# Performance work log

Hardware: AMD Instinct MI355X
Metric: run time of the kernel (lower is better)

Reference implementation:

```python
import jax, jax.numpy as jnp
import numpy as np

DATA_NUM = 1024
CLS_NUM = 32000


def setup_inputs() -> dict:
    key = jax.random.key(0)
    k1, k2, k3, k4 = jax.random.split(key, 4)
    h1 = jax.random.normal(k1, (DATA_NUM, 2), dtype=jnp.float32) + 3.0
    e1 = jax.random.normal(k2, (CLS_NUM, 2), dtype=jnp.float32)
    h3 = jax.random.normal(k3, (DATA_NUM, 2), dtype=jnp.float32) * 2.0
    e3 = jax.random.normal(k4, (CLS_NUM, 2), dtype=jnp.float32)
    return {"h1": h1, "e1": e1, "h3": h3, "e3": e3, "share_head": 0}


def cal_akl(l1, l2):
    # l1: student logits (D, C); l2: teacher logits (D, C)
    probs1 = jax.nn.softmax(l1, axis=-1)
    probs2 = jax.nn.softmax(l2, axis=-1)
    # sort teacher probs ascending; gather student probs in same order
    sorted_idx = jnp.argsort(probs2, axis=-1)
    sorted_probs2 = jnp.take_along_axis(probs2, sorted_idx, axis=-1)
    sorted_probs1 = jnp.take_along_axis(probs1, sorted_idx, axis=-1)
    gap = jnp.abs(sorted_probs2 - sorted_probs1)
    cum_probs2 = jnp.cumsum(sorted_probs2, axis=-1)
    tail_mask = (cum_probs2 < 0.5).astype(l1.dtype)
    g_head = jax.lax.stop_gradient(jnp.sum(gap * (1.0 - tail_mask), axis=-1))
    g_tail = jax.lax.stop_gradient(jnp.sum(gap * tail_mask, axis=-1))
    lprobs1 = jax.nn.log_softmax(l1, axis=-1)
    lprobs2 = jax.nn.log_softmax(l2, axis=-1)
    fkl = jnp.sum(probs2 * (lprobs2 - lprobs1), axis=-1)
    rkl = jnp.sum(probs1 * (lprobs1 - lprobs2), axis=-1)
    denom = g_head + g_tail
    akl = (g_head / denom) * fkl + (g_tail / denom) * rkl
    return jnp.mean(akl)


def reference(h1, e1, h3, e3, share_head):
    # share_head is a static Python int/bool; obj == 'akl', share_head == 0 path
    if share_head:
        raise NotImplementedError("reference covers share_head=False path")
    stu_logits = h1 @ e1.T   # (D, C)
    tea_logits = h3 @ e3.T   # (D, C)
    return cal_akl(stu_logits, tea_logits)
```

## Files before the change

### kernel.cpp

```cpp
#include <hip/hip_runtime.h>
#include <math.h>

#define DNUM 1024
#define CNUM 32000
#define NT 512
#define R 2
#define GRID (DNUM / R)
#define KC 4
#define KF 8
#define NQ (CNUM / 4)
#define NFULL (NQ / NT)
#define TAILN (NQ - NFULL*NT)

#define L2E 1.4426950408889634f
#define LN2 0.6931471805599453f

typedef float v2f __attribute__((ext_vector_type(2)));

__device__ __forceinline__ v2f splat2(float s) { v2f v; v.x = s; v.y = s; return v; }

__device__ __forceinline__ float wave_red_sum(float v) {
    #pragma unroll
    for (int o = 32; o > 0; o >>= 1) v += __shfl_down(v, o, 64);
    return v;
}

__global__ __launch_bounds__(NT, 4) void akl_rows(
    const float* __restrict__ h1, const float* __restrict__ e1,
    const float* __restrict__ h3, const float* __restrict__ e3,
    float* __restrict__ out)
{
    const int tid  = threadIdx.x;
    const int lane = tid & 63, wid = tid >> 6;
    const int row0 = blockIdx.x * R;

    __shared__ float pool[16384];
    __shared__ float red[48];
    __shared__ float shCS[R*KC];
    __shared__ float shFP[R*KF], shFG[R*KF];
    __shared__ float shA[R][7];

    float a1L[R], b1L[R], a2L[R], b2L[R], mh1L[R], mh2L[R], icwC[R], c0C[R];
    #pragma unroll
    for (int r = 0; r < R; r++) {
        a1L[r] = h1[2*(row0+r)] * L2E; b1L[r] = h1[2*(row0+r)+1] * L2E;
        a2L[r] = h3[2*(row0+r)] * L2E; b2L[r] = h3[2*(row0+r)+1] * L2E;
        mh1L[r] = 6.0f * (fabsf(a1L[r]) + fabsf(b1L[r]));
        mh2L[r] = 6.0f * (fabsf(a2L[r]) + fabsf(b2L[r]));
        float sp = fmaxf(sqrtf(a2L[r]*a2L[r] + b2L[r]*b2L[r]), 1e-6f);
        icwC[r] = 1.0f / (1.35f * sp);
        c0C[r] = 0.5f/1.35f + mh2L[r]*icwC[r];
    }
    for (int i = tid; i < 16384; i += NT) pool[i] = 0.f;
    __syncthreads();

    const float4* __restrict__ E1 = (const float4*)e1;
    const float4* __restrict__ E3 = (const float4*)e3;

    v2f U1v[R], S1v[R], S2v[R];
    #pragma unroll
    for (int r = 0; r < R; r++) { U1v[r] = splat2(0.f); S1v[r] = splat2(0.f); S2v[r] = splat2(0.f); }

    auto body1 = [&](int j) {
        float4 A0 = E1[2*j], A1 = E1[2*j+1], B0 = E3[2*j], B1 = E3[2*j+1];
        #pragma unroll
        for (int r = 0; r < R; r++) {
            const v2f a1v = splat2(a1L[r]), b1v = splat2(b1L[r]);
            const v2f a2v = splat2(a2L[r]), b2v = splat2(b2L[r]);
            const v2f m1v = splat2(-mh1L[r]), m2v = splat2(-mh2L[r]);
            const v2f icv = splat2(icwC[r]), c0v = splat2(c0C[r]);
            #pragma unroll
            for (int p = 0; p < 2; p++) {
                float4 A = p ? A1 : A0, B = p ? B1 : B0;
                v2f X1; X1.x = A.x; X1.y = A.z;
                v2f Y1; Y1.x = A.y; Y1.y = A.w;
                v2f X3; X3.x = B.x; X3.y = B.z;
                v2f Y3; Y3.x = B.y; Y3.y = B.w;
                v2f l1 = a1v*X1 + (b1v*Y1 + m1v);
                v2f l2 = a2v*X3 + (b2v*Y3 + m2v);
                v2f e1v; e1v.x = __builtin_amdgcn_exp2f(l1.x);
                         e1v.y = __builtin_amdgcn_exp2f(l1.y);
                v2f e2v; e2v.x = __builtin_amdgcn_exp2f(l2.x);
                         e2v.y = __builtin_amdgcn_exp2f(l2.y);
                v2f dp = l2 - l1;
                U1v[r] += e1v;
                S1v[r] += e1v * dp;
                S2v[r] += e2v * dp;
                v2f t = l2*icv + c0v;
                float t0 = fminf(fmaxf(t.x, 0.f), 3.f);
                float t1 = fminf(fmaxf(t.y, 0.f), 3.f);
                int b0 = (int)t0, b1i = (int)t1;
                float* H0 = pool + (r*4 + 2*p    )*2048;
                float* H1 = pool + (r*4 + 2*p + 1)*2048;
                H0[b0*NT + tid]  += e2v.x;
                H1[b1i*NT + tid] += e2v.y;
            }
        }
    };
    #pragma unroll 1
    for (int it = 0; it < NFULL; ++it) body1(it*NT + tid);
    if (tid < TAILN) body1(NFULL*NT + tid);

    #pragma unroll
    for (int r = 0; r < R; r++) {
        float u = wave_red_sum(U1v[r].x + U1v[r].y);
        float s1 = wave_red_sum(S1v[r].x + S1v[r].y);
        float s2 = wave_red_sum(S2v[r].x + S2v[r].y);
        if (lane == 0) {
            red[wid*6 + r*3 + 0] = u;
            red[wid*6 + r*3 + 1] = s1;
            red[wid*6 + r*3 + 2] = s2;
        }
    }
    __syncthreads();

    {
        int grp = tid >> 6, l = tid & 63;
        int r = grp >> 2, b = grp & 3;
        float s = 0.f;
        #pragma unroll
        for (int c = 0; c < 4; c++) {
            const float* H = pool + (r*4 + c)*2048 + b*512;
            #pragma unroll
            for (int t = 0; t < 8; t++) s += H[l + t*64];
        }
        s = wave_red_sum(s);
        if (l == 0) shCS[grp] = s;
    }
    __syncthreads();

    if (tid < R) {
        const int r = tid;
        float U1s = 0, S1s = 0, S2s = 0;
        for (int w = 0; w < 8; w++) {
            U1s += red[w*6 + r*3 + 0];
            S1s += red[w*6 + r*3 + 1];
            S2s += red[w*6 + r*3 + 2];
        }
        float U2s = 0.f;
        #pragma unroll
        for (int i = 0; i < KC; i++) U2s += shCS[r*KC + i];
        float mh1r = r ? mh1L[1] : mh1L[0];
        float mh2r = r ? mh2L[1] : mh2L[0];
        float a2r = r ? a2L[1] : a2L[0];
        float b2r = r ? b2L[1] : b2L[0];
        float dmh = mh2r - mh1r;
        S1s += dmh * U1s;
        S2s += dmh * U2s;
        float M1 = mh1r + __builtin_amdgcn_logf(U1s);
        float M2 = mh2r + __builtin_amdgcn_logf(U2s);
        float delta = M2 - M1;
        float thr = 0.5f * U2s;
        float S = 0.f; int bsel = KC-1;
        for (int i = 0; i < KC; i++) {
            float m = shCS[r*KC + i];
            if (S + m >= thr) { bsel = i; break; }
            S += m;
        }
        float sp = fmaxf(sqrtf(a2r*a2r + b2r*b2r), 1e-6f);
        float wc  = 1.35f * sp;
        float loS_s = fmaf((float)bsel, wc, -0.5f*sp) - mh2r;
        float icwF = (float)KF / wc;
        shA[r][0] = U2s / U1s;
        shA[r][1] = thr;
        shA[r][2] = LN2 * (S2s/U2s - delta);
        shA[r][3] = LN2 * (delta - S1s/U1s);
        shA[r][4] = icwF;
        shA[r][5] = -loS_s * icwF;
        shA[r][6] = S;
    }
    for (int i = tid; i < 16384; i += NT) pool[i] = 0.f;
    __syncthreads();

    float cR[R], icwFl[R], c0Fl[R];
    #pragma unroll
    for (int r = 0; r < R; r++) {
        cR[r] = shA[r][0]; icwFl[r] = shA[r][4]; c0Fl[r] = shA[r][5];
    }
    v2f gtv[R], Gpv[R];
    #pragma unroll
    for (int r = 0; r < R; r++) { gtv[r] = splat2(0.f); Gpv[r] = splat2(0.f); }

    auto body2 = [&](int j) {
        float4 A0 = E1[2*j], A1 = E1[2*j+1], B0 = E3[2*j], B1 = E3[2*j+1];
        #pragma unroll
        for (int r = 0; r < R; r++) {
            const v2f a1v = splat2(a1L[r]), b1v = splat2(b1L[r]);
            const v2f a2v = splat2(a2L[r]), b2v = splat2(b2L[r]);
            const v2f m1v = splat2(-mh1L[r]), m2v = splat2(-mh2L[r]);
            const v2f cv = splat2(-cR[r]);
            const v2f icv = splat2(icwFl[r]), c0v = splat2(c0Fl[r]);
            float* HP = pool + r*4096;
            float* HG = pool + (2+r)*4096;
            #pragma unroll
            for (int p = 0; p < 2; p++) {
                float4 A = p ? A1 : A0, B = p ? B1 : B0;
                v2f X1; X1.x = A.x; X1.y = A.z;
                v2f Y1; Y1.x = A.y; Y1.y = A.w;
                v2f X3; X3.x = B.x; X3.y = B.z;
                v2f Y3; Y3.x = B.y; Y3.y = B.w;
                v2f l1 = a1v*X1 + (b1v*Y1 + m1v);
                v2f l2 = a2v*X3 + (b2v*Y3 + m2v);
                v2f e1v; e1v.x = __builtin_amdgcn_exp2f(l1.x);
                         e1v.y = __builtin_amdgcn_exp2f(l1.y);
                v2f e2v; e2v.x = __builtin_amdgcn_exp2f(l2.x);
                         e2v.y = __builtin_amdgcn_exp2f(l2.y);
                v2f d = cv*e1v + e2v;
                v2f gap; gap.x = fabsf(d.x); gap.y = fabsf(d.y);
                gtv[r] += gap;
                v2f t = l2*icv + c0v;
                Gpv[r].x += (t.x < 0.f) ? gap.x : 0.f;
                Gpv[r].y += (t.y < 0.f) ? gap.y : 0.f;
                if (t.x >= 0.f && t.x < (float)KF) {
                    int fb = (int)t.x;
                    HP[fb*NT + tid] += e2v.x;
                    HG[fb*NT + tid] += gap.x;
                }
                if (t.y >= 0.f && t.y < (float)KF) {
                    int fb = (int)t.y;
                    HP[fb*NT + tid] += e2v.y;
                    HG[fb*NT + tid] += gap.y;
                }
            }
        }
    };
    #pragma unroll 1
    for (int it = 0; it < NFULL; ++it) body2(it*NT + tid);
    if (tid < TAILN) body2(NFULL*NT + tid);

    #pragma unroll
    for (int r = 0; r < R; r++) {
        float a = wave_red_sum(gtv[r].x + gtv[r].y);
        float b = wave_red_sum(Gpv[r].x + Gpv[r].y);
        if (lane == 0) { red[wid*4 + r*2 + 0] = a; red[wid*4 + r*2 + 1] = b; }
    }
    __syncthreads();

    {
        int grp = tid >> 4, l16 = tid & 15;
        int isG = grp >> 4;
        int r = (grp >> 3) & 1, b = grp & 7;
        const float* H = pool + (isG*2 + r)*4096 + b*512;
        float s = 0.f;
        #pragma unroll
        for (int t = 0; t < NT/16; t++) s += H[l16 + t*16];
        #pragma unroll
        for (int o = 8; o > 0; o >>= 1) s += __shfl_down(s, o, 64);
        if (l16 == 0) {
            if (isG) shFG[r*KF + b] = s; else shFP[r*KF + b] = s;
        }
    }
    __syncthreads();

    if (tid < R) {
        const int r = tid;
        float gts = 0, Gp = 0;
        for (int w = 0; w < 8; w++) {
            gts += red[w*4 + r*2 + 0];
            Gp  += red[w*4 + r*2 + 1];
        }
        float thr = shA[r][1], fkl = shA[r][2], rkl = shA[r][3];
        float S = shA[r][6], G = Gp;
        bool done = false;
        #pragma unroll
        for (int i = 0; i < KF; i++) {
            if (!done) {
                float p = shFP[r*KF + i], g = shFG[r*KF + i];
                float ns = S + p;
                if (ns >= thr) {
                    float f = (thr - S) / fmaxf(p, 1e-30f);
                    f = fminf(fmaxf(f, 0.f), 1.f);
                    G += f * g;
                    done = true;
                } else { S = ns; G += g; }
            }
        }
        float gl = G;
        float gh = gts - gl;
        float akl = (gh*fkl + gl*rkl) / gts;
        unsafeAtomicAdd(out, akl * (1.0f/(float)DNUM));
    }
}

extern "C" void kernel_launch(void* const* d_in, const int* in_sizes, int n_in,
                              void* d_out, int out_size, void* d_ws, size_t ws_size,
                              hipStream_t stream) {
    const float* h1 = (const float*)d_in[0];
    const float* e1 = (const float*)d_in[1];
    const float* h3 = (const float*)d_in[2];
    const float* e3 = (const float*)d_in[3];
    hipMemsetAsync(d_out, 0, sizeof(float), stream);
    akl_rows<<<GRID, NT, 0, stream>>>(h1, e1, h3, e3, (float*)d_out);
}
```

Measured before the change: 107.1 us.

## Process one row per block instead of two, halving LDS and raising occupancy

Each block now handles a single data row instead of two, so the grid doubles to one block per row. Shared-memory histograms shrink from 64KB to 32KB and launch bounds rise to allow more resident blocks per CU. The tail iteration is folded into the main loop count. The cost is that the e1/e3 class tables are streamed twice as many times overall, since the two rows no longer share each load.

```diff
diff --git a/kernel.cpp b/kernel.cpp
--- a/kernel.cpp
+++ b/kernel.cpp
@@ -4,8 +4,7 @@
 #define DNUM 1024
 #define CNUM 32000
 #define NT 512
-#define R 2
-#define GRID (DNUM / R)
+#define GRID DNUM
 #define KC 4
 #define KF 8
 #define NQ (CNUM / 4)
@@ -25,50 +24,49 @@
     return v;
 }
 
-__global__ __launch_bounds__(NT, 4) void akl_rows(
+__global__ __launch_bounds__(NT, 8) void akl_rows(
     const float* __restrict__ h1, const float* __restrict__ e1,
     const float* __restrict__ h3, const float* __restrict__ e3,
     float* __restrict__ out)
 {
     const int tid  = threadIdx.x;
     const int lane = tid & 63, wid = tid >> 6;
-    const int row0 = blockIdx.x * R;
-
-    __shared__ float pool[16384];
-    __shared__ float red[48];
-    __shared__ float shCS[R*KC];
-    __shared__ float shFP[R*KF], shFG[R*KF];
-    __shared__ float shA[R][7];
-
-    float a1L[R], b1L[R], a2L[R], b2L[R], mh1L[R], mh2L[R], icwC[R], c0C[R];
-    #pragma unroll
-    for (int r = 0; r < R; r++) {
-        a1L[r] = h1[2*(row0+r)] * L2E; b1L[r] = h1[2*(row0+r)+1] * L2E;
-        a2L[r] = h3[2*(row0+r)] * L2E; b2L[r] = h3[2*(row0+r)+1] * L2E;
-        mh1L[r] = 6.0f * (fabsf(a1L[r]) + fabsf(b1L[r]));
-        mh2L[r] = 6.0f * (fabsf(a2L[r]) + fabsf(b2L[r]));
-        float sp = fmaxf(sqrtf(a2L[r]*a2L[r] + b2L[r]*b2L[r]), 1e-6f);
-        icwC[r] = 1.0f / (1.35f * sp);
-        c0C[r] = 0.5f/1.35f + mh2L[r]*icwC[r];
-    }
-    for (int i = tid; i < 16384; i += NT) pool[i] = 0.f;
+    const int row = blockIdx.x;
+
+    __shared__ float pool[8192];
+    __shared__ float red[24];
+    __shared__ float shCS[KC];
+    __shared__ float shFP[KF], shFG[KF];
+    __shared__ float shA[7];
+
+    const float a1L = h1[2*row] * L2E,  b1L = h1[2*row+1] * L2E;
+    const float a2L = h3[2*row] * L2E,  b2L = h3[2*row+1] * L2E;
+    const float mh1L = 6.0f * (fabsf(a1L) + fabsf(b1L));
+    const float mh2L = 6.0f * (fabsf(a2L) + fabsf(b2L));
+    const float spC = fmaxf(sqrtf(a2L*a2L + b2L*b2L), 1e-6f);
+    const float icwC = 1.0f / (1.35f * spC);
+    const float c0C = 0.5f/1.35f + mh2L*icwC;
+
+    for (int i = tid; i < 8192; i += NT) pool[i] = 0.f;
     __syncthreads();
 
     const float4* __restrict__ E1 = (const float4*)e1;
     const float4* __restrict__ E3 = (const float4*)e3;
 
-    v2f U1v[R], S1v[R], S2v[R];
-    #pragma unroll
-    for (int r = 0; r < R; r++) { U1v[r] = splat2(0.f); S1v[r] = splat2(0.f); S2v[r] = splat2(0.f); }
-
-    auto body1 = [&](int j) {
-        float4 A0 = E1[2*j], A1 = E1[2*j+1], B0 = E3[2*j], B1 = E3[2*j+1];
-        #pragma unroll
-        for (int r = 0; r < R; r++) {
-            const v2f a1v = splat2(a1L[r]), b1v = splat2(b1L[r]);
-            const v2f a2v = splat2(a2L[r]), b2v = splat2(b2L[r]);
-            const v2f m1v = splat2(-mh1L[r]), m2v = splat2(-mh2L[r]);
-            const v2f icv = splat2(icwC[r]), c0v = splat2(c0C[r]);
+    const int cnt = NFULL + ((tid < TAILN) ? 1 : 0);
+
+    v2f U1v = splat2(0.f), S1v = splat2(0.f), S2v = splat2(0.f);
+
+    {
+        const v2f a1v = splat2(a1L), b1v = splat2(b1L);
+        const v2f a2v = splat2(a2L), b2v = splat2(b2L);
+        const v2f m1v = splat2(-mh1L), m2v = splat2(-mh2L);
+        const v2f icv = splat2(icwC), c0v = splat2(c0C);
+        #pragma unroll 1
+        for (int it = 0; it < cnt; ++it) {
+            const int j = it*NT + tid;
+            float4 A0 = E1[2*j], A1 = E1[2*j+1];
+            float4 B0 = E3[2*j], B1 = E3[2*j+1];
             #pragma unroll
             for (int p = 0; p < 2; p++) {
                 float4 A = p ? A1 : A0, B = p ? B1 : B0;
@@ -83,115 +81,100 @@
                 v2f e2v; e2v.x = __builtin_amdgcn_exp2f(l2.x);
                          e2v.y = __builtin_amdgcn_exp2f(l2.y);
                 v2f dp = l2 - l1;
-                U1v[r] += e1v;
-                S1v[r] += e1v * dp;
-                S2v[r] += e2v * dp;
+                U1v += e1v;
+                S1v += e1v * dp;
+                S2v += e2v * dp;
                 v2f t = l2*icv + c0v;
                 float t0 = fminf(fmaxf(t.x, 0.f), 3.f);
                 float t1 = fminf(fmaxf(t.y, 0.f), 3.f);
                 int b0 = (int)t0, b1i = (int)t1;
-                float* H0 = pool + (r*4 + 2*p    )*2048;
-                float* H1 = pool + (r*4 + 2*p + 1)*2048;
+                float* H0 = pool + (2*p    )*2048;
+                float* H1 = pool + (2*p + 1)*2048;
                 H0[b0*NT + tid]  += e2v.x;
                 H1[b1i*NT + tid] += e2v.y;
             }
         }
-    };
-    #pragma unroll 1
-    for (int it = 0; it < NFULL; ++it) body1(it*NT + tid);
-    if (tid < TAILN) body1(NFULL*NT + tid);
-
-    #pragma unroll
-    for (int r = 0; r < R; r++) {
-        float u = wave_red_sum(U1v[r].x + U1v[r].y);
-        float s1 = wave_red_sum(S1v[r].x + S1v[r].y);
-        float s2 = wave_red_sum(S2v[r].x + S2v[r].y);
+    }
+
+    {
+        float u  = wave_red_sum(U1v.x + U1v.y);
+        float s1 = wave_red_sum(S1v.x + S1v.y);
+        float s2 = wave_red_sum(S2v.x + S2v.y);
         if (lane == 0) {
-            red[wid*6 + r*3 + 0] = u;
-            red[wid*6 + r*3 + 1] = s1;
-            red[wid*6 + r*3 + 2] = s2;
-        }
-    }
-    __syncthreads();
-
-    {
-        int grp = tid >> 6, l = tid & 63;
-        int r = grp >> 2, b = grp & 3;
+            red[wid*3 + 0] = u;
+            red[wid*3 + 1] = s1;
+            red[wid*3 + 2] = s2;
+        }
+    }
+    __syncthreads();
+
+    if (tid < 256) {
+        int b = tid >> 6, l = tid & 63;
         float s = 0.f;
         #pragma unroll
         for (int c = 0; c < 4; c++) {
-            const float* H = pool + (r*4 + c)*2048 + b*512;
+            const float* H = pool + c*2048 + b*512;
             #pragma unroll
             for (int t = 0; t < 8; t++) s += H[l + t*64];
         }
         s = wave_red_sum(s);
-        if (l == 0) shCS[grp] = s;
-    }
-    __syncthreads();
-
-    if (tid < R) {
-        const int r = tid;
+        if (l == 0) shCS[b] = s;
+    }
+    __syncthreads();
+
+    if (tid == 0) {
         float U1s = 0, S1s = 0, S2s = 0;
         for (int w = 0; w < 8; w++) {
-            U1s += red[w*6 + r*3 + 0];
-            S1s += red[w*6 + r*3 + 1];
-            S2s += red[w*6 + r*3 + 2];
+            U1s += red[w*3 + 0];
+            S1s += red[w*3 + 1];
+            S2s += red[w*3 + 2];
         }
         float U2s = 0.f;
         #pragma unroll
-        for (int i = 0; i < KC; i++) U2s += shCS[r*KC + i];
-        float mh1r = r ? mh1L[1] : mh1L[0];
-        float mh2r = r ? mh2L[1] : mh2L[0];
-        float a2r = r ? a2L[1] : a2L[0];
-        float b2r = r ? b2L[1] : b2L[0];
-        float dmh = mh2r - mh1r;
+        for (int i = 0; i < KC; i++) U2s += shCS[i];
+        float dmh = mh2L - mh1L;
         S1s += dmh * U1s;
         S2s += dmh * U2s;
-        float M1 = mh1r + __builtin_amdgcn_logf(U1s);
-        float M2 = mh2r + __builtin_amdgcn_logf(U2s);
+        float M1 = mh1L + __builtin_amdgcn_logf(U1s);
+        float M2 = mh2L + __builtin_amdgcn_logf(U2s);
         float delta = M2 - M1;
         float thr = 0.5f * U2s;
         float S = 0.f; int bsel = KC-1;
         for (int i = 0; i < KC; i++) {
-            float m = shCS[r*KC + i];
+            float m = shCS[i];
             if (S + m >= thr) { bsel = i; break; }
             S += m;
         }
-        float sp = fmaxf(sqrtf(a2r*a2r + b2r*b2r), 1e-6f);
-        float wc  = 1.35f * sp;
-        float loS_s = fmaf((float)bsel, wc, -0.5f*sp) - mh2r;
+        float wc  = 1.35f * spC;
+        float loS_s = fmaf((float)bsel, wc, -0.5f*spC) - mh2L;
         float icwF = (float)KF / wc;
-        shA[r][0] = U2s / U1s;
-        shA[r][1] = thr;
-        shA[r][2] = LN2 * (S2s/U2s - delta);
-        shA[r][3] = LN2 * (delta - S1s/U1s);
-        shA[r][4] = icwF;
-        shA[r][5] = -loS_s * icwF;
-        shA[r][6] = S;
-    }
-    for (int i = tid; i < 16384; i += NT) pool[i] = 0.f;
-    __syncthreads();
-
-    float cR[R], icwFl[R], c0Fl[R];
-    #pragma unroll
-    for (int r = 0; r < R; r++) {
-        cR[r] = shA[r][0]; icwFl[r] = shA[r][4]; c0Fl[r] = shA[r][5];
-    }
-    v2f gtv[R], Gpv[R];
-    #pragma unroll
-    for (int r = 0; r < R; r++) { gtv[r] = splat2(0.f); Gpv[r] = splat2(0.f); }
-
-    auto body2 = [&](int j) {
-        float4 A0 = E1[2*j], A1 = E1[2*j+1], B0 = E3[2*j], B1 = E3[2*j+1];
-        #pragma unroll
-        for (int r = 0; r < R; r++) {
-            const v2f a1v = splat2(a1L[r]), b1v = splat2(b1L[r]);
-            const v2f a2v = splat2(a2L[r]), b2v = splat2(b2L[r]);
-            const v2f m1v = splat2(-mh1L[r]), m2v = splat2(-mh2L[r]);
-            const v2f cv = splat2(-cR[r]);
-            const v2f icv = splat2(icwFl[r]), c0v = splat2(c0Fl[r]);
-            float* HP = pool + r*4096;
-            float* HG = pool + (2+r)*4096;
+        shA[0] = U2s / U1s;
+        shA[1] = thr;
+        shA[2] = LN2 * (S2s/U2s - delta);
+        shA[3] = LN2 * (delta - S1s/U1s);
+        shA[4] = icwF;
+        shA[5] = -loS_s * icwF;
+        shA[6] = S;
+    }
+    for (int i = tid; i < 8192; i += NT) pool[i] = 0.f;
+    __syncthreads();
+
+    const float cR = shA[0], icwF = shA[4], c0F = shA[5];
+    v2f gtv = splat2(0.f), Gpv = splat2(0.f);
+
+    {
+        const v2f a1v = splat2(a1L), b1v = splat2(b1L);
+        const v2f a2v = splat2(a2L), b2v = splat2(b2L);
+        const v2f m1v = splat2(-mh1L), m2v = splat2(-mh2L);
+        const v2f cv = splat2(-cR);
+        const v2f icv = splat2(icwF), c0v = splat2(c0F);
+        float* HP = pool;
+        float* HG = pool + 4096;
+        #pragma unroll 1
+        for (int it = 0; it < cnt; ++it) {
+            const int j = it*NT + tid;
+            float4 A0 = E1[2*j], A1 = E1[2*j+1];
+            float4 B0 = E3[2*j], B1 = E3[2*j+1];
             #pragma unroll
             for (int p = 0; p < 2; p++) {
                 float4 A = p ? A1 : A0, B = p ? B1 : B0;
@@ -207,10 +190,10 @@
                          e2v.y = __builtin_amdgcn_exp2f(l2.y);
                 v2f d = cv*e1v + e2v;
                 v2f gap; gap.x = fabsf(d.x); gap.y = fabsf(d.y);
-                gtv[r] += gap;
+                gtv += gap;
                 v2f t = l2*icv + c0v;
-                Gpv[r].x += (t.x < 0.f) ? gap.x : 0.f;
-                Gpv[r].y += (t.y < 0.f) ? gap.y : 0.f;
+                Gpv.x += (t.x < 0.f) ? gap.x : 0.f;
+                Gpv.y += (t.y < 0.f) ? gap.y : 0.f;
                 if (t.x >= 0.f && t.x < (float)KF) {
                     int fb = (int)t.x;
                     HP[fb*NT + tid] += e2v.x;
@@ -223,49 +206,43 @@
                 }
             }
         }
-    };
-    #pragma unroll 1
-    for (int it = 0; it < NFULL; ++it) body2(it*NT + tid);
-    if (tid < TAILN) body2(NFULL*NT + tid);
-
-    #pragma unroll
-    for (int r = 0; r < R; r++) {
-        float a = wave_red_sum(gtv[r].x + gtv[r].y);
-        float b = wave_red_sum(Gpv[r].x + Gpv[r].y);
-        if (lane == 0) { red[wid*4 + r*2 + 0] = a; red[wid*4 + r*2 + 1] = b; }
-    }
-    __syncthreads();
-
-    {
-        int grp = tid >> 4, l16 = tid & 15;
-        int isG = grp >> 4;
-        int r = (grp >> 3) & 1, b = grp & 7;
-        const float* H = pool + (isG*2 + r)*4096 + b*512;
+    }
+
+    {
+        float a = wave_red_sum(gtv.x + gtv.y);
+        float b = wave_red_sum(Gpv.x + Gpv.y);
+        if (lane == 0) { red[wid*2 + 0] = a; red[wid*2 + 1] = b; }
+    }
+    __syncthreads();
+
+    {
+        int grp = tid >> 5, l32 = tid & 31;
+        int isG = grp >> 3, b = grp & 7;
+        const float* H = pool + isG*4096 + b*512;
         float s = 0.f;
         #pragma unroll
-        for (int t = 0; t < NT/16; t++) s += H[l16 + t*16];
-        #pragma unroll
-        for (int o = 8; o > 0; o >>= 1) s += __shfl_down(s, o, 64);
-        if (l16 == 0) {
-            if (isG) shFG[r*KF + b] = s; else shFP[r*KF + b] = s;
-        }
-    }
-    __syncthreads();
-
-    if (tid < R) {
-        const int r = tid;
+        for (int t = 0; t < NT/32; t++) s += H[l32 + t*32];
+        #pragma unroll
+        for (int o = 16; o > 0; o >>= 1) s += __shfl_down(s, o, 32);
+        if (l32 == 0) {
+            if (isG) shFG[b] = s; else shFP[b] = s;
+        }
+    }
+    __syncthreads();
+
+    if (tid == 0) {
         float gts = 0, Gp = 0;
         for (int w = 0; w < 8; w++) {
-            gts += red[w*4 + r*2 + 0];
-            Gp  += red[w*4 + r*2 + 1];
-        }
-        float thr = shA[r][1], fkl = shA[r][2], rkl = shA[r][3];
-        float S = shA[r][6], G = Gp;
+            gts += red[w*2 + 0];
+            Gp  += red[w*2 + 1];
+        }
+        float thr = shA[1], fkl = shA[2], rkl = shA[3];
+        float S = shA[6], G = Gp;
         bool done = false;
         #pragma unroll
         for (int i = 0; i < KF; i++) {
             if (!done) {
-                float p = shFP[r*KF + i], g = shFG[r*KF + i];
+                float p = shFP[i], g = shFG[i];
                 float ns = S + p;
                 if (ns >= thr) {
                     float f = (thr - S) / fmaxf(p, 1e-30f);
```

After: 110.3 us. 1.03x slower.

## Double block size to 1024 threads and rebalance coarse/fine histogram bins

Applied to the files above, without the earlier changes.

Raises threads per block from 512 to 1024 so each block covers its two rows with more parallel lanes, and reshapes the per-thread LDS histograms to fit the larger block. The coarse pass now uses 8 narrower bins and the fine pass 4, and the duplicated per-parity histograms are merged into one per row, so two lanes now add into the same histogram. The aim is more memory-level parallelism per block and fewer iterations per thread. The risk is that occupancy stays limited by the 64KB LDS pool, and there is more barrier and reduction work per block.

```diff
diff --git a/kernel.cpp b/kernel.cpp
--- a/kernel.cpp
+++ b/kernel.cpp
@@ -3,11 +3,11 @@
 
 #define DNUM 1024
 #define CNUM 32000
-#define NT 512
+#define NT 1024
 #define R 2
 #define GRID (DNUM / R)
-#define KC 4
-#define KF 8
+#define KC 8
+#define KF 4
 #define NQ (CNUM / 4)
 #define NFULL (NQ / NT)
 #define TAILN (NQ - NFULL*NT)
@@ -25,7 +25,7 @@
     return v;
 }
 
-__global__ __launch_bounds__(NT, 4) void akl_rows(
+__global__ __launch_bounds__(NT, 8) void akl_rows(
     const float* __restrict__ h1, const float* __restrict__ e1,
     const float* __restrict__ h3, const float* __restrict__ e3,
     float* __restrict__ out)
@@ -35,7 +35,7 @@
     const int row0 = blockIdx.x * R;
 
     __shared__ float pool[16384];
-    __shared__ float red[48];
+    __shared__ float red[96];
     __shared__ float shCS[R*KC];
     __shared__ float shFP[R*KF], shFG[R*KF];
     __shared__ float shA[R][7];
@@ -48,8 +48,8 @@
         mh1L[r] = 6.0f * (fabsf(a1L[r]) + fabsf(b1L[r]));
         mh2L[r] = 6.0f * (fabsf(a2L[r]) + fabsf(b2L[r]));
         float sp = fmaxf(sqrtf(a2L[r]*a2L[r] + b2L[r]*b2L[r]), 1e-6f);
-        icwC[r] = 1.0f / (1.35f * sp);
-        c0C[r] = 0.5f/1.35f + mh2L[r]*icwC[r];
+        icwC[r] = 1.0f / (0.675f * sp);
+        c0C[r] = 0.5f/0.675f + mh2L[r]*icwC[r];
     }
     for (int i = tid; i < 16384; i += NT) pool[i] = 0.f;
     __syncthreads();
@@ -57,18 +57,24 @@
     const float4* __restrict__ E1 = (const float4*)e1;
     const float4* __restrict__ E3 = (const float4*)e3;
 
+    const int cnt = NFULL + ((tid < TAILN) ? 1 : 0);
+
     v2f U1v[R], S1v[R], S2v[R];
     #pragma unroll
     for (int r = 0; r < R; r++) { U1v[r] = splat2(0.f); S1v[r] = splat2(0.f); S2v[r] = splat2(0.f); }
 
-    auto body1 = [&](int j) {
-        float4 A0 = E1[2*j], A1 = E1[2*j+1], B0 = E3[2*j], B1 = E3[2*j+1];
+    #pragma unroll 1
+    for (int it = 0; it < cnt; ++it) {
+        const int j = it*NT + tid;
+        float4 A0 = E1[2*j], A1 = E1[2*j+1];
+        float4 B0 = E3[2*j], B1 = E3[2*j+1];
         #pragma unroll
         for (int r = 0; r < R; r++) {
             const v2f a1v = splat2(a1L[r]), b1v = splat2(b1L[r]);
             const v2f a2v = splat2(a2L[r]), b2v = splat2(b2L[r]);
             const v2f m1v = splat2(-mh1L[r]), m2v = splat2(-mh2L[r]);
             const v2f icv = splat2(icwC[r]), c0v = splat2(c0C[r]);
+            float* H = pool + r*8192;
             #pragma unroll
             for (int p = 0; p < 2; p++) {
                 float4 A = p ? A1 : A0, B = p ? B1 : B0;
@@ -87,19 +93,14 @@
                 S1v[r] += e1v * dp;
                 S2v[r] += e2v * dp;
                 v2f t = l2*icv + c0v;
-                float t0 = fminf(fmaxf(t.x, 0.f), 3.f);
-                float t1 = fminf(fmaxf(t.y, 0.f), 3.f);
+                float t0 = fminf(fmaxf(t.x, 0.f), 7.f);
+                float t1 = fminf(fmaxf(t.y, 0.f), 7.f);
                 int b0 = (int)t0, b1i = (int)t1;
-                float* H0 = pool + (r*4 + 2*p    )*2048;
-                float* H1 = pool + (r*4 + 2*p + 1)*2048;
-                H0[b0*NT + tid]  += e2v.x;
-                H1[b1i*NT + tid] += e2v.y;
+                H[b0*NT + tid]  += e2v.x;
+                H[b1i*NT + tid] += e2v.y;
             }
         }
-    };
-    #pragma unroll 1
-    for (int it = 0; it < NFULL; ++it) body1(it*NT + tid);
-    if (tid < TAILN) body1(NFULL*NT + tid);
+    }
 
     #pragma unroll
     for (int r = 0; r < R; r++) {
@@ -115,24 +116,20 @@
     __syncthreads();
 
     {
-        int grp = tid >> 6, l = tid & 63;
-        int r = grp >> 2, b = grp & 3;
+        int r = wid >> 3, b = wid & 7;
+        const float* H = pool + r*8192 + b*NT;
         float s = 0.f;
         #pragma unroll
-        for (int c = 0; c < 4; c++) {
-            const float* H = pool + (r*4 + c)*2048 + b*512;
-            #pragma unroll
-            for (int t = 0; t < 8; t++) s += H[l + t*64];
-        }
+        for (int t = 0; t < NT/64; t++) s += H[lane + t*64];
         s = wave_red_sum(s);
-        if (l == 0) shCS[grp] = s;
+        if (lane == 0) shCS[r*KC + b] = s;
     }
     __syncthreads();
 
     if (tid < R) {
         const int r = tid;
         float U1s = 0, S1s = 0, S2s = 0;
-        for (int w = 0; w < 8; w++) {
+        for (int w = 0; w < 16; w++) {
             U1s += red[w*6 + r*3 + 0];
             S1s += red[w*6 + r*3 + 1];
             S2s += red[w*6 + r*3 + 2];
@@ -158,7 +155,7 @@
             S += m;
         }
         float sp = fmaxf(sqrtf(a2r*a2r + b2r*b2r), 1e-6f);
-        float wc  = 1.35f * sp;
+        float wc  = 0.675f * sp;
         float loS_s = fmaf((float)bsel, wc, -0.5f*sp) - mh2r;
         float icwF = (float)KF / wc;
         shA[r][0] = U2s / U1s;
@@ -181,8 +178,11 @@
     #pragma unroll
     for (int r = 0; r < R; r++) { gtv[r] = splat2(0.f); Gpv[r] = splat2(0.f); }
 
-    auto body2 = [&](int j) {
-        float4 A0 = E1[2*j], A1 = E1[2*j+1], B0 = E3[2*j], B1 = E3[2*j+1];
+    #pragma unroll 1
+    for (int it = 0; it < cnt; ++it) {
+        const int j = it*NT + tid;
+        float4 A0 = E1[2*j], A1 = E1[2*j+1];
+        float4 B0 = E3[2*j], B1 = E3[2*j+1];
         #pragma unroll
         for (int r = 0; r < R; r++) {
             const v2f a1v = splat2(a1L[r]), b1v = splat2(b1L[r]);
@@ -191,7 +191,7 @@
             const v2f cv = splat2(-cR[r]);
             const v2f icv = splat2(icwFl[r]), c0v = splat2(c0Fl[r]);
             float* HP = pool + r*4096;
-            float* HG = pool + (2+r)*4096;
+            float* HG = pool + 8192 + r*4096;
             #pragma unroll
             for (int p = 0; p < 2; p++) {
                 float4 A = p ? A1 : A0, B = p ? B1 : B0;
@@ -223,10 +223,7 @@
                 }
             }
         }
-    };
-    #pragma unroll 1
-    for (int it = 0; it < NFULL; ++it) body2(it*NT + tid);
-    if (tid < TAILN) body2(NFULL*NT + tid);
+    }
 
     #pragma unroll
     for (int r = 0; r < R; r++) {
@@ -237,16 +234,15 @@
     __syncthreads();
 
     {
-        int grp = tid >> 4, l16 = tid & 15;
-        int isG = grp >> 4;
-        int r = (grp >> 3) & 1, b = grp & 7;
-        const float* H = pool + (isG*2 + r)*4096 + b*512;
+        int isG = wid >> 3;
+        int rem = wid & 7;
+        int r = rem >> 2, b = rem & 3;
+        const float* H = pool + isG*8192 + r*4096 + b*NT;
         float s = 0.f;
         #pragma unroll
-        for (int t = 0; t < NT/16; t++) s += H[l16 + t*16];
-        #pragma unroll
-        for (int o = 8; o > 0; o >>= 1) s += __shfl_down(s, o, 64);
-        if (l16 == 0) {
+        for (int t = 0; t < NT/64; t++) s += H[lane + t*64];
+        s = wave_red_sum(s);
+        if (lane == 0) {
             if (isG) shFG[r*KF + b] = s; else shFP[r*KF + b] = s;
         }
     }
@@ -255,7 +251,7 @@
     if (tid < R) {
         const int r = tid;
         float gts = 0, Gp = 0;
-        for (int w = 0; w < 8; w++) {
+        for (int w = 0; w < 16; w++) {
             gts += red[w*4 + r*2 + 0];
             Gp  += red[w*4 + r*2 + 1];
         }
```

Measured after the change: 208.2 us. 1.94x slower.
